# Kernel tuning notes

Measured on AMD Instinct MI355X. Metric: run time of the kernel, lower is better.

Reference implementation:

```python
import jax, jax.numpy as jnp
import numpy as np

B, N, C_IN, C_OUT, K = 4, 4096, 128, 128, 3
EPS = 1e-06
LAMBDA_MAX = 2.0  # compute_lambda_max=False and lambda_max=None -> 2.0


def setup_inputs() -> dict:
    key = jax.random.key(0)
    k1, k2, k3 = jax.random.split(key, 3)
    x = jax.random.normal(k1, (B, N, C_IN), dtype=jnp.float32)
    adj = jax.random.uniform(k2, (B, N, N), dtype=jnp.float32)
    W = jax.random.normal(k3, (C_OUT, K * C_IN), dtype=jnp.float32) * 0.05
    return {"x": x, "adj": adj, "W": W}


def reference(x, adj, W):
    # degree: sum over dim=1 of adj (matches torch adj.sum(dim=1).unsqueeze(-1))
    degree = jnp.sum(adj, axis=1)[:, :, None]          # [B, N, 1]
    lambda_ratio = 2.0 / (LAMBDA_MAX + EPS)

    def cheb_step(z):
        # lr * D * z - lr * A @ z - z, fused elementwise around one bmm
        return lambda_ratio * (degree * z - jnp.einsum('bnm,bmc->bnc', adj, z)) - z

    Z_list = [x, cheb_step(x)]
    for k in range(2, K):
        Z_list.append(2.0 * cheb_step(Z_list[k - 1]) - Z_list[k - 2])

    Z = jnp.stack(Z_list, axis=1)                      # [B, K, N, C]
    # replicate torch .view(B, N, -1) on contiguous [B, K, N, C]
    Z = Z.reshape(Z.shape[0], Z.shape[2], -1)          # [B, N, K*C]
    out = jnp.einsum('bnf,of->bno', Z, W)              # Linear, no bias
    return out
```

## Files before the change

kernel.cpp:

```cpp
#include <hip/hip_runtime.h>


#define NN 4096
#define CF 128
#define NC (NN * CF)
#define LRC 0.9999995f

typedef __attribute__((ext_vector_type(8))) short bf16x8;
typedef __attribute__((ext_vector_type(4))) float f32x4;

__device__ __forceinline__ unsigned short f2b(float f) {
    unsigned u = __float_as_uint(f);
    return (unsigned short)((u + 0x7FFFu + ((u >> 16) & 1u)) >> 16);
}

__global__ __launch_bounds__(256) void prep_cast(const float* __restrict__ adj,
                                                 unsigned short* __restrict__ adjB,
                                                 float* __restrict__ deg) {
    const int b = blockIdx.z;
    const size_t base = (size_t)b * NN * NN;
    const int n0 = blockIdx.x * 1024;
    const int m0 = blockIdx.y * 256;
    const int t = threadIdx.x;
    float4 s = make_float4(0.f, 0.f, 0.f, 0.f);
    const size_t col = (size_t)(n0 + t * 4);
    for (int m = 0; m < 256; ++m) {
        const size_t idx = base + (size_t)(m0 + m) * NN + col;
        const float4 v = *(const float4*)&adj[idx];
        s.x += v.x; s.y += v.y; s.z += v.z; s.w += v.w;
        ushort4 o;
        o.x = f2b(v.x); o.y = f2b(v.y); o.z = f2b(v.z); o.w = f2b(v.w);
        *(ushort4*)&adjB[idx] = o;
    }
    float* dp = deg + b * NN + n0 + t * 4;
    atomicAdd(dp + 0, s.x);
    atomicAdd(dp + 1, s.y);
    atomicAdd(dp + 2, s.z);
    atomicAdd(dp + 3, s.w);
}

__global__ __launch_bounds__(256) void transpose_x(const float* __restrict__ x,
                                                   unsigned short* __restrict__ xTb) {
    __shared__ float tile[64][65];
    const int b = blockIdx.z, m0 = blockIdx.x * 64, n0 = blockIdx.y * 64;
    const int t = threadIdx.x;
    const int c = t & 63, r4 = t >> 6;
    const float* xb = x + (size_t)b * NC;
#pragma unroll
    for (int i = 0; i < 16; ++i) {
        int r = i * 4 + r4;
        tile[r][c] = xb[(size_t)(m0 + r) * CF + n0 + c];
    }
    __syncthreads();
    unsigned short* xo = xTb + (size_t)b * NC + (size_t)n0 * NN + m0;
#pragma unroll
    for (int i = 0; i < 16; ++i) {
        int r = i * 4 + r4;
        xo[(size_t)r * NN + c] = f2b(tile[c][r]);
    }
}

__global__ __launch_bounds__(256) void wt_kernel(const float* __restrict__ W,
                                                 float* __restrict__ Wt) {
    const int idx = blockIdx.x * 256 + threadIdx.x;
    const int o = idx / 384;
    const int f = idx % 384;
    Wt[f * 128 + o] = W[idx];
}

__global__ __launch_bounds__(256, 2) void mfma_part(
    const unsigned short* __restrict__ adjB,
    const unsigned short* __restrict__ Bt,
    float* __restrict__ Cpart)
{
    const int t = threadIdx.x;
    const int w = t >> 6, lane = t & 63, q = lane >> 4, l16 = lane & 15;
    const int wm = w & 1, wn = w >> 1;
    const int m0 = blockIdx.x * 128;
    const int kc = blockIdx.y;
    const int b  = blockIdx.z;

    __shared__ __align__(16) short As[8192];
    __shared__ __align__(16) short Bs[8192];

    const int g  = t & 7;
    const int r0 = t >> 3;

    const unsigned short* ap = adjB + (size_t)b * NN * NN + (size_t)kc * 1024 + g * 8;
    const unsigned short* bp = Bt   + (size_t)b * NC      + (size_t)kc * 1024 + g * 8;

    f32x4 acc[4][4];
#pragma unroll
    for (int i = 0; i < 4; ++i)
#pragma unroll
        for (int j = 0; j < 4; ++j) acc[i][j] = (f32x4)0.f;

    bf16x8 ar[4], br[4];
#pragma unroll
    for (int i = 0; i < 4; ++i) {
        const int r = r0 + i * 32;
        ar[i] = *(const bf16x8*)(ap + (size_t)(m0 + r) * NN);
        br[i] = *(const bf16x8*)(bp + (size_t)r * NN);
    }

    for (int it = 0; it < 16; ++it) {
        __syncthreads();
#pragma unroll
        for (int i = 0; i < 4; ++i) {
            const int r = r0 + i * 32;
            const int slot = (g ^ (r & 7)) << 3;
            *(bf16x8*)&As[r * 64 + slot] = ar[i];
            *(bf16x8*)&Bs[r * 64 + slot] = br[i];
        }
        __syncthreads();
        if (it < 15) {
            const int kof = (it + 1) * 64;
#pragma unroll
            for (int i = 0; i < 4; ++i) {
                const int r = r0 + i * 32;
                ar[i] = *(const bf16x8*)(ap + (size_t)(m0 + r) * NN + kof);
                br[i] = *(const bf16x8*)(bp + (size_t)r * NN + kof);
            }
        }
#pragma unroll
        for (int kh = 0; kh < 2; ++kh) {
            bf16x8 af[4], bf[4];
#pragma unroll
            for (int i = 0; i < 4; ++i) {
                const int ml = wm * 64 + i * 16 + l16;
                af[i] = *(const bf16x8*)&As[ml * 64 + ((((kh << 2) + q) ^ (ml & 7)) << 3)];
                const int nl = wn * 64 + i * 16 + l16;
                bf[i] = *(const bf16x8*)&Bs[nl * 64 + ((((kh << 2) + q) ^ (nl & 7)) << 3)];
            }
#pragma unroll
            for (int i = 0; i < 4; ++i)
#pragma unroll
                for (int j = 0; j < 4; ++j)
                    acc[i][j] = __builtin_amdgcn_mfma_f32_16x16x32_bf16(
                        af[i], bf[j], acc[i][j], 0, 0, 0);
        }
    }

    float* Cb = Cpart + (size_t)(b * 4 + kc) * NC;
#pragma unroll
    for (int i = 0; i < 4; ++i) {
        const int mrow = m0 + wm * 64 + i * 16 + q * 4;
#pragma unroll
        for (int j = 0; j < 4; ++j) {
            const int n = wn * 64 + j * 16 + l16;
#pragma unroll
            for (int r = 0; r < 4; ++r)
                Cb[(size_t)(mrow + r) * CF + n] = acc[i][j][r];
        }
    }
}

__global__ __launch_bounds__(256) void reduce_z1(const float* __restrict__ Cpart,
                                                 const float* __restrict__ x,
                                                 const float* __restrict__ deg,
                                                 float* __restrict__ Zf,
                                                 unsigned short* __restrict__ z1Tb) {
    __shared__ unsigned short sh[64][68];
    const int b = blockIdx.z, m0 = blockIdx.x * 64, n0 = blockIdx.y * 64;
    const int t = threadIdx.x;
    const int r0 = (t >> 4) * 4, c0 = (t & 15) * 4;
    const float* degb = deg + b * NN;
    const float* xb = x + (size_t)b * NC;
    float* Zf1 = Zf + (size_t)b * 2 * NC;
#pragma unroll
    for (int rr = 0; rr < 4; ++rr) {
        const int m = m0 + r0 + rr;
        f32x4 s = (f32x4)0.f;
#pragma unroll
        for (int kc = 0; kc < 4; ++kc)
            s += *(const f32x4*)&Cpart[(size_t)(b * 4 + kc) * NC + (size_t)m * CF + n0 + c0];
        const f32x4 xv = *(const f32x4*)&xb[(size_t)m * CF + n0 + c0];
        const float d = degb[m];
        f32x4 z;
#pragma unroll
        for (int cc = 0; cc < 4; ++cc) z[cc] = LRC * (d * xv[cc] - s[cc]) - xv[cc];
        *(f32x4*)&Zf1[(size_t)m * CF + n0 + c0] = z;
#pragma unroll
        for (int cc = 0; cc < 4; ++cc) sh[c0 + cc][r0 + rr] = f2b(z[cc]);
    }
    __syncthreads();
    unsigned short* zo = z1Tb + (size_t)b * NC + (size_t)n0 * NN + m0;
    const int nl = t >> 2;
#pragma unroll
    for (int i = 0; i < 4; ++i) {
        const int ml = ((t & 3) + i * 4) * 4;
        ushort4 v;
        v.x = sh[nl][ml]; v.y = sh[nl][ml + 1]; v.z = sh[nl][ml + 2]; v.w = sh[nl][ml + 3];
        *(ushort4*)&zo[(size_t)nl * NN + ml] = v;
    }
}

__global__ __launch_bounds__(256) void reduce_z2(const float* __restrict__ Cpart,
                                                 const float* __restrict__ x,
                                                 const float* __restrict__ deg,
                                                 float* __restrict__ Zf) {
    const size_t gidx = (size_t)blockIdx.x * 256 + threadIdx.x;
    const int b = (int)(gidx / (NC / 4));
    const size_t rem = gidx % (NC / 4);
    const int m = (int)(rem / (CF / 4));
    const int c0 = (int)(rem % (CF / 4)) * 4;
    f32x4 s = (f32x4)0.f;
#pragma unroll
    for (int kc = 0; kc < 4; ++kc)
        s += *(const f32x4*)&Cpart[(size_t)(b * 4 + kc) * NC + (size_t)m * CF + c0];
    const f32x4 xv = *(const f32x4*)&x[(size_t)b * NC + (size_t)m * CF + c0];
    const f32x4 z1 = *(const f32x4*)&Zf[(size_t)b * 2 * NC + (size_t)m * CF + c0];
    const float d = deg[b * NN + m];
    f32x4 z;
#pragma unroll
    for (int cc = 0; cc < 4; ++cc)
        z[cc] = 2.f * (LRC * (d * z1[cc] - s[cc]) - z1[cc]) - xv[cc];
    *(f32x4*)&Zf[(size_t)b * 2 * NC + NC + (size_t)m * CF + c0] = z;
}

__global__ __launch_bounds__(256) void gemm_final(const float* __restrict__ x,
                                                  const float* __restrict__ Zf,
                                                  const float* __restrict__ Wt,
                                                  float* __restrict__ out) {
    const int b = blockIdx.z;
    float* Cb = out + (size_t)b * NC;

    const int t = threadIdx.x;
    const int tx = t & 15, ty = t >> 4;
    const int m0 = blockIdx.y * 64, n0 = blockIdx.x * 64;

    __shared__ float Asm[16][68];
    __shared__ float Bsm[16][64];

    const int arow = t >> 2;
    const int ak4 = (t & 3) << 2;
    const int bk = t >> 4;
    const int bn4 = (t & 15) << 2;

    const float* xb = x + (size_t)b * NC;

    float4 acc[4];
    acc[0] = acc[1] = acc[2] = acc[3] = make_float4(0.f, 0.f, 0.f, 0.f);

    const float* bptr = Wt + (size_t)bk * 128 + n0 + bn4;

    auto aload = [&](int k) -> float4 {
        const unsigned G = (unsigned)(m0 + arow) * 384u + (unsigned)k;
        const int chunk = (int)(G >> 19);
        const unsigned rem = G & 524287u;
        const float* src = (chunk == 0) ? xb : (Zf + (size_t)(b * 2 + (chunk - 1)) * NC);
        return *(const float4*)&src[rem];
    };

    float4 av = aload(ak4);
    float4 bv = *(const float4*)bptr;

    for (int k0 = 0; k0 < 384; k0 += 16) {
        __syncthreads();
        Asm[ak4 + 0][arow] = av.x;
        Asm[ak4 + 1][arow] = av.y;
        Asm[ak4 + 2][arow] = av.z;
        Asm[ak4 + 3][arow] = av.w;
        *(float4*)&Bsm[bk][bn4] = bv;
        __syncthreads();
        if (k0 + 16 < 384) {
            av = aload(k0 + 16 + ak4);
            bv = *(const float4*)(bptr + (size_t)(k0 + 16) * 128);
        }
#pragma unroll
        for (int kk = 0; kk < 16; ++kk) {
            const float4 a = *(const float4*)&Asm[kk][ty << 2];
            const float4 bb = *(const float4*)&Bsm[kk][tx << 2];
            acc[0].x += a.x * bb.x; acc[0].y += a.x * bb.y; acc[0].z += a.x * bb.z; acc[0].w += a.x * bb.w;
            acc[1].x += a.y * bb.x; acc[1].y += a.y * bb.y; acc[1].z += a.y * bb.z; acc[1].w += a.y * bb.w;
            acc[2].x += a.z * bb.x; acc[2].y += a.z * bb.y; acc[2].z += a.z * bb.z; acc[2].w += a.z * bb.w;
            acc[3].x += a.w * bb.x; acc[3].y += a.w * bb.y; acc[3].z += a.w * bb.z; acc[3].w += a.w * bb.w;
        }
    }

    const int ncol = n0 + (tx << 2);
#pragma unroll
    for (int i = 0; i < 4; ++i) {
        const int m = m0 + (ty << 2) + i;
        *(float4*)&Cb[(size_t)m * 128 + ncol] = acc[i];
    }
}

extern "C" void kernel_launch(void* const* d_in, const int* in_sizes, int n_in,
                              void* d_out, int out_size, void* d_ws, size_t ws_size,
                              hipStream_t stream) {
    const float* x   = (const float*)d_in[0];
    const float* adj = (const float*)d_in[1];
    const float* W   = (const float*)d_in[2];
    float* out = (float*)d_out;

    char* ws = (char*)d_ws;
    unsigned short* adjB = (unsigned short*)ws;
    float* Cpart         = (float*)(ws + 134217728u);
    float* Zf            = (float*)(ws + 167772160u);
    unsigned short* xTb  = (unsigned short*)(ws + 184549376u);
    unsigned short* z1Tb = (unsigned short*)(ws + 188743680u);
    float* deg           = (float*)(ws + 192937984u);
    float* Wt            = (float*)(ws + 193003520u);

    hipMemsetAsync(deg, 0, 4 * NN * sizeof(float), stream);
    prep_cast<<<dim3(4, 16, 4), 256, 0, stream>>>(adj, adjB, deg);
    transpose_x<<<dim3(64, 2, 4), 256, 0, stream>>>(x, xTb);
    wt_kernel<<<192, 256, 0, stream>>>(W, Wt);

    mfma_part<<<dim3(32, 4, 4), 256, 0, stream>>>(adjB, xTb, Cpart);
    reduce_z1<<<dim3(64, 2, 4), 256, 0, stream>>>(Cpart, x, deg, Zf, z1Tb);

    mfma_part<<<dim3(32, 4, 4), 256, 0, stream>>>(adjB, z1Tb, Cpart);
    reduce_z2<<<2048, 256, 0, stream>>>(Cpart, x, deg, Zf);

    gemm_final<<<dim3(2, 64, 4), 256, 0, stream>>>(x, Zf, Wt, out);
}
```

Before: 512.3 us.

## Drop split-K in adjacency GEMMs and fuse Chebyshev epilogue into them

The adjacency GEMM no longer splits K into four partial buffers. Each block now computes a 64-row by 128-column tile over the full K range, using double-buffered shared memory, and applies the Chebyshev update (plus the bf16 transpose for Z1) in its epilogue. This removes the Cpart write/read round trips and two reduce kernels, and prep_cast gets a finer grid. In exchange the GEMM launches only 256 blocks with long serial K loops, which may underfill the GPU and lose latency hiding.

```diff
diff --git a/kernel.cpp b/kernel.cpp
--- a/kernel.cpp
+++ b/kernel.cpp
@@ -20,11 +20,11 @@
     const int b = blockIdx.z;
     const size_t base = (size_t)b * NN * NN;
     const int n0 = blockIdx.x * 1024;
-    const int m0 = blockIdx.y * 256;
+    const int m0 = blockIdx.y * 64;
     const int t = threadIdx.x;
     float4 s = make_float4(0.f, 0.f, 0.f, 0.f);
     const size_t col = (size_t)(n0 + t * 4);
-    for (int m = 0; m < 256; ++m) {
+    for (int m = 0; m < 64; ++m) {
         const size_t idx = base + (size_t)(m0 + m) * NN + col;
         const float4 v = *(const float4*)&adj[idx];
         s.x += v.x; s.y += v.y; s.z += v.z; s.w += v.w;
@@ -68,154 +68,150 @@
     Wt[f * 128 + o] = W[idx];
 }
 
-__global__ __launch_bounds__(256, 2) void mfma_part(
+template <int PHASE>
+__global__ __launch_bounds__(256) void gemm_cheb(
     const unsigned short* __restrict__ adjB,
     const unsigned short* __restrict__ Bt,
-    float* __restrict__ Cpart)
+    const float* __restrict__ x,
+    const float* __restrict__ deg,
+    float* __restrict__ Zf,
+    unsigned short* __restrict__ z1Tb)
 {
     const int t = threadIdx.x;
     const int w = t >> 6, lane = t & 63, q = lane >> 4, l16 = lane & 15;
-    const int wm = w & 1, wn = w >> 1;
-    const int m0 = blockIdx.x * 128;
-    const int kc = blockIdx.y;
-    const int b  = blockIdx.z;
-
-    __shared__ __align__(16) short As[8192];
-    __shared__ __align__(16) short Bs[8192];
+    const int m0 = blockIdx.x * 64;
+    const int b  = blockIdx.y;
+
+    __shared__ __align__(16) short As[2][4096];
+    __shared__ __align__(16) short Bs[2][8192];
 
     const int g  = t & 7;
     const int r0 = t >> 3;
 
-    const unsigned short* ap = adjB + (size_t)b * NN * NN + (size_t)kc * 1024 + g * 8;
-    const unsigned short* bp = Bt   + (size_t)b * NC      + (size_t)kc * 1024 + g * 8;
-
-    f32x4 acc[4][4];
+    const unsigned short* ap = adjB + (size_t)b * NN * NN + (size_t)m0 * NN + g * 8;
+    const unsigned short* bp = Bt   + (size_t)b * NC + g * 8;
+
+    f32x4 acc[4][2];
 #pragma unroll
     for (int i = 0; i < 4; ++i)
 #pragma unroll
-        for (int j = 0; j < 4; ++j) acc[i][j] = (f32x4)0.f;
-
-    bf16x8 ar[4], br[4];
-#pragma unroll
-    for (int i = 0; i < 4; ++i) {
-        const int r = r0 + i * 32;
-        ar[i] = *(const bf16x8*)(ap + (size_t)(m0 + r) * NN);
-        br[i] = *(const bf16x8*)(bp + (size_t)r * NN);
-    }
-
-    for (int it = 0; it < 16; ++it) {
-        __syncthreads();
+        for (int j = 0; j < 2; ++j) acc[i][j] = (f32x4)0.f;
+
+    bf16x8 ar[2], br[4];
+    ar[0] = *(const bf16x8*)(ap + (size_t)r0 * NN);
+    ar[1] = *(const bf16x8*)(ap + (size_t)(r0 + 32) * NN);
+#pragma unroll
+    for (int i = 0; i < 4; ++i)
+        br[i] = *(const bf16x8*)(bp + (size_t)(r0 + 32 * i) * NN);
+
+    {
+        const int ra = r0, rb = r0 + 32;
+        *(bf16x8*)&As[0][ra * 64 + ((g ^ (ra & 7)) << 3)] = ar[0];
+        *(bf16x8*)&As[0][rb * 64 + ((g ^ (rb & 7)) << 3)] = ar[1];
 #pragma unroll
         for (int i = 0; i < 4; ++i) {
-            const int r = r0 + i * 32;
-            const int slot = (g ^ (r & 7)) << 3;
-            *(bf16x8*)&As[r * 64 + slot] = ar[i];
-            *(bf16x8*)&Bs[r * 64 + slot] = br[i];
-        }
-        __syncthreads();
-        if (it < 15) {
-            const int kof = (it + 1) * 64;
+            const int r = r0 + 32 * i;
+            *(bf16x8*)&Bs[0][r * 64 + ((g ^ (r & 7)) << 3)] = br[i];
+        }
+    }
+
+    int cur = 0;
+    for (int it = 0; it < 64; ++it) {
+        __syncthreads();
+        if (it < 63) {
+            const size_t kof = (size_t)(it + 1) * 64;
+            ar[0] = *(const bf16x8*)(ap + (size_t)r0 * NN + kof);
+            ar[1] = *(const bf16x8*)(ap + (size_t)(r0 + 32) * NN + kof);
+#pragma unroll
+            for (int i = 0; i < 4; ++i)
+                br[i] = *(const bf16x8*)(bp + (size_t)(r0 + 32 * i) * NN + kof);
+        }
+#pragma unroll
+        for (int kh = 0; kh < 2; ++kh) {
+            bf16x8 af[4], bfr[2];
 #pragma unroll
             for (int i = 0; i < 4; ++i) {
-                const int r = r0 + i * 32;
-                ar[i] = *(const bf16x8*)(ap + (size_t)(m0 + r) * NN + kof);
-                br[i] = *(const bf16x8*)(bp + (size_t)r * NN + kof);
-            }
-        }
-#pragma unroll
-        for (int kh = 0; kh < 2; ++kh) {
-            bf16x8 af[4], bf[4];
+                const int ml = i * 16 + l16;
+                af[i] = *(const bf16x8*)&As[cur][ml * 64 + ((((kh << 2) + q) ^ (ml & 7)) << 3)];
+            }
+#pragma unroll
+            for (int j = 0; j < 2; ++j) {
+                const int nl = w * 32 + j * 16 + l16;
+                bfr[j] = *(const bf16x8*)&Bs[cur][nl * 64 + ((((kh << 2) + q) ^ (nl & 7)) << 3)];
+            }
+#pragma unroll
+            for (int i = 0; i < 4; ++i)
+#pragma unroll
+                for (int j = 0; j < 2; ++j)
+                    acc[i][j] = __builtin_amdgcn_mfma_f32_16x16x32_bf16(
+                        af[i], bfr[j], acc[i][j], 0, 0, 0);
+        }
+        if (it < 63) {
+            const int nxt = cur ^ 1;
+            const int ra = r0, rb = r0 + 32;
+            *(bf16x8*)&As[nxt][ra * 64 + ((g ^ (ra & 7)) << 3)] = ar[0];
+            *(bf16x8*)&As[nxt][rb * 64 + ((g ^ (rb & 7)) << 3)] = ar[1];
 #pragma unroll
             for (int i = 0; i < 4; ++i) {
-                const int ml = wm * 64 + i * 16 + l16;
-                af[i] = *(const bf16x8*)&As[ml * 64 + ((((kh << 2) + q) ^ (ml & 7)) << 3)];
-                const int nl = wn * 64 + i * 16 + l16;
-                bf[i] = *(const bf16x8*)&Bs[nl * 64 + ((((kh << 2) + q) ^ (nl & 7)) << 3)];
-            }
-#pragma unroll
-            for (int i = 0; i < 4; ++i)
-#pragma unroll
-                for (int j = 0; j < 4; ++j)
-                    acc[i][j] = __builtin_amdgcn_mfma_f32_16x16x32_bf16(
-                        af[i], bf[j], acc[i][j], 0, 0, 0);
-        }
-    }
-
-    float* Cb = Cpart + (size_t)(b * 4 + kc) * NC;
-#pragma unroll
-    for (int i = 0; i < 4; ++i) {
-        const int mrow = m0 + wm * 64 + i * 16 + q * 4;
-#pragma unroll
-        for (int j = 0; j < 4; ++j) {
-            const int n = wn * 64 + j * 16 + l16;
-#pragma unroll
-            for (int r = 0; r < 4; ++r)
-                Cb[(size_t)(mrow + r) * CF + n] = acc[i][j][r];
-        }
-    }
-}
-
-__global__ __launch_bounds__(256) void reduce_z1(const float* __restrict__ Cpart,
-                                                 const float* __restrict__ x,
-                                                 const float* __restrict__ deg,
-                                                 float* __restrict__ Zf,
-                                                 unsigned short* __restrict__ z1Tb) {
-    __shared__ unsigned short sh[64][68];
-    const int b = blockIdx.z, m0 = blockIdx.x * 64, n0 = blockIdx.y * 64;
-    const int t = threadIdx.x;
-    const int r0 = (t >> 4) * 4, c0 = (t & 15) * 4;
+                const int r = r0 + 32 * i;
+                *(bf16x8*)&Bs[nxt][r * 64 + ((g ^ (r & 7)) << 3)] = br[i];
+            }
+            cur = nxt;
+        }
+    }
+
+    const float* xb   = x + (size_t)b * NC;
     const float* degb = deg + b * NN;
-    const float* xb = x + (size_t)b * NC;
-    float* Zf1 = Zf + (size_t)b * 2 * NC;
-#pragma unroll
-    for (int rr = 0; rr < 4; ++rr) {
-        const int m = m0 + r0 + rr;
-        f32x4 s = (f32x4)0.f;
-#pragma unroll
-        for (int kc = 0; kc < 4; ++kc)
-            s += *(const f32x4*)&Cpart[(size_t)(b * 4 + kc) * NC + (size_t)m * CF + n0 + c0];
-        const f32x4 xv = *(const f32x4*)&xb[(size_t)m * CF + n0 + c0];
-        const float d = degb[m];
-        f32x4 z;
-#pragma unroll
-        for (int cc = 0; cc < 4; ++cc) z[cc] = LRC * (d * xv[cc] - s[cc]) - xv[cc];
-        *(f32x4*)&Zf1[(size_t)m * CF + n0 + c0] = z;
-#pragma unroll
-        for (int cc = 0; cc < 4; ++cc) sh[c0 + cc][r0 + rr] = f2b(z[cc]);
-    }
-    __syncthreads();
-    unsigned short* zo = z1Tb + (size_t)b * NC + (size_t)n0 * NN + m0;
-    const int nl = t >> 2;
-#pragma unroll
-    for (int i = 0; i < 4; ++i) {
-        const int ml = ((t & 3) + i * 4) * 4;
-        ushort4 v;
-        v.x = sh[nl][ml]; v.y = sh[nl][ml + 1]; v.z = sh[nl][ml + 2]; v.w = sh[nl][ml + 3];
-        *(ushort4*)&zo[(size_t)nl * NN + ml] = v;
-    }
-}
-
-__global__ __launch_bounds__(256) void reduce_z2(const float* __restrict__ Cpart,
-                                                 const float* __restrict__ x,
-                                                 const float* __restrict__ deg,
-                                                 float* __restrict__ Zf) {
-    const size_t gidx = (size_t)blockIdx.x * 256 + threadIdx.x;
-    const int b = (int)(gidx / (NC / 4));
-    const size_t rem = gidx % (NC / 4);
-    const int m = (int)(rem / (CF / 4));
-    const int c0 = (int)(rem % (CF / 4)) * 4;
-    f32x4 s = (f32x4)0.f;
-#pragma unroll
-    for (int kc = 0; kc < 4; ++kc)
-        s += *(const f32x4*)&Cpart[(size_t)(b * 4 + kc) * NC + (size_t)m * CF + c0];
-    const f32x4 xv = *(const f32x4*)&x[(size_t)b * NC + (size_t)m * CF + c0];
-    const f32x4 z1 = *(const f32x4*)&Zf[(size_t)b * 2 * NC + (size_t)m * CF + c0];
-    const float d = deg[b * NN + m];
-    f32x4 z;
-#pragma unroll
-    for (int cc = 0; cc < 4; ++cc)
-        z[cc] = 2.f * (LRC * (d * z1[cc] - s[cc]) - z1[cc]) - xv[cc];
-    *(f32x4*)&Zf[(size_t)b * 2 * NC + NC + (size_t)m * CF + c0] = z;
+    float* Z1 = Zf + (size_t)b * 2 * NC;
+
+    if (PHASE == 0) {
+        __syncthreads();
+        short (*sh)[68] = (short(*)[68])(&Bs[0][0]);
+#pragma unroll
+        for (int i = 0; i < 4; ++i) {
+#pragma unroll
+            for (int r = 0; r < 4; ++r) {
+                const int ml = i * 16 + q * 4 + r;
+                const int m  = m0 + ml;
+                const float d = degb[m];
+#pragma unroll
+                for (int j = 0; j < 2; ++j) {
+                    const int n = w * 32 + j * 16 + l16;
+                    const float xv = xb[(size_t)m * CF + n];
+                    const float zz = LRC * (d * xv - acc[i][j][r]) - xv;
+                    Z1[(size_t)m * CF + n] = zz;
+                    sh[n][ml] = (short)f2b(zz);
+                }
+            }
+        }
+        __syncthreads();
+        const int f  = t >> 1;
+        const int h0 = (t & 1) * 32;
+        unsigned short* zo = z1Tb + (size_t)b * NC + (size_t)f * NN + m0 + h0;
+        const short* srow = &sh[f][h0];
+#pragma unroll
+        for (int v = 0; v < 8; ++v)
+            ((ushort4*)zo)[v] = ((const ushort4*)srow)[v];
+    } else {
+        const float* Z1c = Z1;
+        float* Z2 = Z1 + NC;
+#pragma unroll
+        for (int i = 0; i < 4; ++i) {
+#pragma unroll
+            for (int r = 0; r < 4; ++r) {
+                const int m = m0 + i * 16 + q * 4 + r;
+                const float d = degb[m];
+#pragma unroll
+                for (int j = 0; j < 2; ++j) {
+                    const int n = w * 32 + j * 16 + l16;
+                    const float xv  = xb[(size_t)m * CF + n];
+                    const float z1v = Z1c[(size_t)m * CF + n];
+                    Z2[(size_t)m * CF + n] =
+                        2.f * (LRC * (d * z1v - acc[i][j][r]) - z1v) - xv;
+                }
+            }
+        }
+    }
 }
 
 __global__ __launch_bounds__(256) void gemm_final(const float* __restrict__ x,
@@ -296,23 +292,19 @@
 
     char* ws = (char*)d_ws;
     unsigned short* adjB = (unsigned short*)ws;
-    float* Cpart         = (float*)(ws + 134217728u);
-    float* Zf            = (float*)(ws + 167772160u);
-    unsigned short* xTb  = (unsigned short*)(ws + 184549376u);
-    unsigned short* z1Tb = (unsigned short*)(ws + 188743680u);
-    float* deg           = (float*)(ws + 192937984u);
-    float* Wt            = (float*)(ws + 193003520u);
+    float* Zf            = (float*)(ws + 134217728u);
+    unsigned short* xTb  = (unsigned short*)(ws + 150994944u);
+    unsigned short* z1Tb = (unsigned short*)(ws + 155189248u);
+    float* deg           = (float*)(ws + 159383552u);
+    float* Wt            = (float*)(ws + 159449088u);
 
     hipMemsetAsync(deg, 0, 4 * NN * sizeof(float), stream);
-    prep_cast<<<dim3(4, 16, 4), 256, 0, stream>>>(adj, adjB, deg);
+    prep_cast<<<dim3(4, 64, 4), 256, 0, stream>>>(adj, adjB, deg);
     transpose_x<<<dim3(64, 2, 4), 256, 0, stream>>>(x, xTb);
     wt_kernel<<<192, 256, 0, stream>>>(W, Wt);
 
-    mfma_part<<<dim3(32, 4, 4), 256, 0, stream>>>(adjB, xTb, Cpart);
-    reduce_z1<<<dim3(64, 2, 4), 256, 0, stream>>>(Cpart, x, deg, Zf, z1Tb);
-
-    mfma_part<<<dim3(32, 4, 4), 256, 0, stream>>>(adjB, z1Tb, Cpart);
-    reduce_z2<<<2048, 256, 0, stream>>>(Cpart, x, deg, Zf);
+    gemm_cheb<0><<<dim3(64, 4), 256, 0, stream>>>(adjB, xTb, x, deg, Zf, z1Tb);
+    gemm_cheb<1><<<dim3(64, 4), 256, 0, stream>>>(adjB, z1Tb, x, deg, Zf, z1Tb);
 
     gemm_final<<<dim3(2, 64, 4), 256, 0, stream>>>(x, Zf, Wt, out);
 }
```

Measured after the change: 544.0 us. 6.2% more time.
